# Optimization experiments

Hardware: AMD Instinct MI355X
Metric: run time of the kernel (lower is better)

Reference implementation:

```python
import jax, jax.numpy as jnp
import numpy as np

HID, HEADS, LAYERS = 64, 4, 2
D = HID // HEADS
NU, NE, NV = 30000, 60000, 1000
N_NODES = (NU, NE, NV)
OFFS = (0, NU, NU + NE, NU + NE + NV)
N_TOTAL = NU + NE + NV
# (src_type, dst_type, n_edges); node types: user=0, event=1, venue=2. Order matches module.edge_types.
EDGE_DEFS = (
    (0, 0, 150000),  # friend
    (0, 1, 120000), (0, 1, 60000), (0, 1, 40000), (0, 1, 30000), (0, 1, 50000),  # view/like/save/intent/attend
    (1, 0, 120000), (1, 0, 60000), (1, 0, 40000), (1, 0, 30000), (1, 0, 50000),  # rev_*
    (1, 2, 60000),  # hosted_at
    (2, 1, 60000),  # hosts
)
EDGE_NAMES = ('ei_friend', 'ei_view', 'ei_like', 'ei_save', 'ei_intent', 'ei_attend',
              'ei_rev_view', 'ei_rev_like', 'ei_rev_save', 'ei_rev_intent', 'ei_rev_attend',
              'ei_hosted_at', 'ei_hosts')


def _l2norm(x):
    return x / jnp.maximum(jnp.linalg.norm(x, axis=-1, keepdims=True), 1e-12)


def _hgt_layer(h, edges, Wkqv, bkqv, Wk, Wv, p_rel, Wout, bout, skip):
    # h: list of per-node-type features [N_t, HID]. Fused K/Q/V projection per node type.
    kqv = [h[t] @ Wkqv[t] + bkqv[t] for t in range(3)]  # [N_t, 3*HID]
    k = [a[:, :HID].reshape(-1, HEADS, D) for a in kqv]
    q = [a[:, HID:2 * HID].reshape(-1, HEADS, D) for a in kqv]
    v = [a[:, 2 * HID:].reshape(-1, HEADS, D) for a in kqv]
    scale = 1.0 / np.sqrt(D).astype(np.float32)
    scores, msgs, dsts = [], [], []
    for e, (s, d, _) in enumerate(EDGE_DEFS):
        src_idx, dst_idx = edges[e][0], edges[e][1]
        # per-(edge_type, head) DxD relation transforms (PyG k_rel / v_rel)
        ke = jnp.einsum('nhd,hde->nhe', k[s], Wk[e])[src_idx]  # [E,H,D]
        ve = jnp.einsum('nhd,hde->nhe', v[s], Wv[e])[src_idx]  # [E,H,D]
        qi = q[d][dst_idx]                                      # [E,H,D]
        scores.append((qi * ke).sum(-1) * p_rel[e] * scale)     # [E,H]
        msgs.append(ve)
        dsts.append(dst_idx + OFFS[d])
    sc = jnp.concatenate(scores)   # [E_tot, H]
    ms = jnp.concatenate(msgs)     # [E_tot, H, D]
    dst = jnp.concatenate(dsts)    # [E_tot] global destination ids
    # destination-grouped softmax across all edge types jointly
    smax = jax.lax.stop_gradient(jax.ops.segment_max(sc, dst, num_segments=N_TOTAL))
    ex = jnp.exp(sc - smax[dst])
    den = jax.ops.segment_sum(ex, dst, num_segments=N_TOTAL)
    alpha = ex / den[dst]
    agg = jax.ops.segment_sum(alpha[:, :, None] * ms, dst, num_segments=N_TOTAL).reshape(N_TOTAL, HID)
    out = []
    for t in range(3):
        o = agg[OFFS[t]:OFFS[t + 1]]
        a = jax.nn.gelu(o, approximate=False) @ Wout[t] + bout[t]
        g = jax.nn.sigmoid(skip[t])  # learnable skip gate
        out.append(g * a + (1.0 - g) * h[t])
    return out


def _forward(x_user, x_event, x_venue, W_user, b_user, W_event, b_event, W_venue, b_venue,
             emb_user, emb_event, emb_venue, Wkqv, bkqv, Wk, Wv, p_rel, Wout, bout, skip,
             ids_user, ids_event, ids_venue, edges):
    h = [x_user @ W_user + b_user + emb_user[ids_user],
         x_event @ W_event + b_event + emb_event[ids_event],
         x_venue @ W_venue + b_venue + emb_venue[ids_venue]]
    for l in range(LAYERS):
        h = _hgt_layer(h, edges, Wkqv[l], bkqv[l], Wk[l], Wv[l], p_rel[l], Wout[l], bout[l], skip[l])
        h = [jax.nn.relu(x) for x in h]  # dropout is identity in eval mode
    return tuple(_l2norm(x) for x in h)


def setup_inputs() -> dict:
    key = jax.random.key(0)
    ks = iter(jax.random.split(key, 64))
    s = 0.05
    inp = {
        'x_user': jax.random.normal(next(ks), (NU, 32), jnp.float32),
        'x_event': jax.random.normal(next(ks), (NE, 32), jnp.float32),
        'x_venue': jax.random.normal(next(ks), (NV, 16), jnp.float32),
        'W_user': jax.random.normal(next(ks), (32, HID), jnp.float32) * s,
        'b_user': jnp.zeros((HID,), jnp.float32),
        'W_event': jax.random.normal(next(ks), (32, HID), jnp.float32) * s,
        'b_event': jnp.zeros((HID,), jnp.float32),
        'W_venue': jax.random.normal(next(ks), (16, HID), jnp.float32) * s,
        'b_venue': jnp.zeros((HID,), jnp.float32),
        'emb_user': jax.random.normal(next(ks), (NU, HID), jnp.float32) * s,
        'emb_event': jax.random.normal(next(ks), (NE, HID), jnp.float32) * s,
        'emb_venue': jax.random.normal(next(ks), (NV, HID), jnp.float32) * s,
        'Wkqv': jax.random.normal(next(ks), (LAYERS, 3, HID, 3 * HID), jnp.float32) * s,
        'bkqv': jnp.zeros((LAYERS, 3, 3 * HID), jnp.float32),
        'Wk': jax.random.normal(next(ks), (LAYERS, 13, HEADS, D, D), jnp.float32) * 0.2,
        'Wv': jax.random.normal(next(ks), (LAYERS, 13, HEADS, D, D), jnp.float32) * 0.2,
        'p_rel': jnp.ones((LAYERS, 13, HEADS), jnp.float32),
        'Wout': jax.random.normal(next(ks), (LAYERS, 3, HID, HID), jnp.float32) * s,
        'bout': jnp.zeros((LAYERS, 3, HID), jnp.float32),
        'skip': jnp.ones((LAYERS, 3), jnp.float32),
        'ids_user': jnp.arange(NU, dtype=jnp.int32),
        'ids_event': jnp.arange(NE, dtype=jnp.int32),
        'ids_venue': jnp.arange(NV, dtype=jnp.int32),
    }
    for name, (st, dt, n) in zip(EDGE_NAMES, EDGE_DEFS):
        src = jax.random.randint(next(ks), (n,), 0, N_NODES[st], dtype=jnp.int32)
        dst = jax.random.randint(next(ks), (n,), 0, N_NODES[dt], dtype=jnp.int32)
        inp[name] = jnp.stack([src, dst])
    return inp


def reference(x_user, x_event, x_venue, W_user, b_user, W_event, b_event, W_venue, b_venue,
              emb_user, emb_event, emb_venue, Wkqv, bkqv, Wk, Wv, p_rel, Wout, bout, skip,
              ids_user, ids_event, ids_venue,
              ei_friend, ei_view, ei_like, ei_save, ei_intent, ei_attend,
              ei_rev_view, ei_rev_like, ei_rev_save, ei_rev_intent, ei_rev_attend,
              ei_hosted_at, ei_hosts):
    edges = (ei_friend, ei_view, ei_like, ei_save, ei_intent, ei_attend,
             ei_rev_view, ei_rev_like, ei_rev_save, ei_rev_intent, ei_rev_attend,
             ei_hosted_at, ei_hosts)
    return _forward(x_user, x_event, x_venue, W_user, b_user, W_event, b_event, W_venue, b_venue,
                    emb_user, emb_event, emb_venue, Wkqv, bkqv, Wk, Wv, p_rel, Wout, bout, skip,
                    ids_user, ids_event, ids_venue, edges)
```

## Files before the change

kernel.cpp:

```cpp
#include <hip/hip_runtime.h>
#include <hip/hip_fp16.h>
#include <math.h>

#define HID   64
#define HEADS 4
#define DH    16
#define NU    30000
#define NE_   60000
#define NV    1000
#define NTOT  91000
#define ETOT  870000
#define NSLOT 541000
#define LAYERS 2

__device__ const int d_EOFF[14] = {0,150000,270000,330000,370000,400000,450000,
                                   570000,630000,670000,700000,750000,810000,870000};
__device__ const int d_ECNT[13] = {150000,120000,60000,40000,30000,50000,
                                   120000,60000,40000,30000,50000,60000,60000};
__device__ const int d_EST[13]  = {0,0,0,0,0,0,1,1,1,1,1,1,2};
__device__ const int d_EDT[13]  = {0,1,1,1,1,1,0,0,0,0,0,2,1};
__device__ const int d_NOFF[3]  = {0, NU, NU + NE_};
__device__ const int d_EBASE[13] = {0,30000,60000,90000,120000,150000,
                                    180000,240000,300000,360000,420000,480000,540000};

struct EdgePtrs { const int* p[13]; };

typedef float f32x2 __attribute__((ext_vector_type(2)));

__device__ __forceinline__ void pk_fma(f32x2& acc, f32x2 a, f32x2 b) {
    asm("v_pk_fma_f32 %0, %1, %2, %0" : "+v"(acc) : "v"(a), "v"(b));
}

__device__ __forceinline__ int node_type(int n) {
    return (n >= NU) + (n >= NU + NE_);
}

__global__ void k_init(const float* __restrict__ xu, const float* __restrict__ xe,
                       const float* __restrict__ xv,
                       const float* __restrict__ Wu, const float* __restrict__ bu,
                       const float* __restrict__ We, const float* __restrict__ be,
                       const float* __restrict__ Wv_, const float* __restrict__ bv,
                       const float* __restrict__ embu, const float* __restrict__ embe,
                       const float* __restrict__ embv,
                       const int* __restrict__ idu, const int* __restrict__ ide,
                       const int* __restrict__ idv,
                       float* __restrict__ h) {
    int gid = blockIdx.x * blockDim.x + threadIdx.x;
    if (gid >= NTOT * HID) return;
    int node = gid >> 6, j = gid & 63;
    const float *x, *W, *b, *emb; const int* ids; int in_dim, n;
    if (node < NU)            { n = node;           x = xu; W = Wu;  b = bu; emb = embu; ids = idu; in_dim = 32; }
    else if (node < NU + NE_) { n = node - NU;      x = xe; W = We;  b = be; emb = embe; ids = ide; in_dim = 32; }
    else                      { n = node - NU - NE_;x = xv; W = Wv_; b = bv; emb = embv; ids = idv; in_dim = 16; }
    float acc = b[j] + emb[(size_t)ids[n] * HID + j];
    for (int i = 0; i < in_dim; i++) acc += x[(size_t)n * in_dim + i] * W[i * HID + j];
    h[gid] = acc;
}

__global__ void k_cnt(EdgePtrs ep, int* __restrict__ cnt) {
    int eidx = blockIdx.x * blockDim.x + threadIdx.x;
    if (eidx >= ETOT) return;
    int e = 0;
    #pragma unroll
    for (int i = 1; i < 13; i++) e += (eidx >= d_EOFF[i]);
    int li = eidx - d_EOFF[e];
    int dst = ep.p[e][d_ECNT[e] + li];
    atomicAdd(&cnt[d_NOFF[d_EDT[e]] + dst], 1);
}

__global__ void k_scan_a(const int* __restrict__ cnt, int* __restrict__ partial) {
    __shared__ int s[256];
    int i = blockIdx.x * 256 + threadIdx.x;
    s[threadIdx.x] = (i < NTOT) ? cnt[i] : 0;
    __syncthreads();
    for (int off = 128; off > 0; off >>= 1) {
        if (threadIdx.x < off) s[threadIdx.x] += s[threadIdx.x + off];
        __syncthreads();
    }
    if (threadIdx.x == 0) partial[blockIdx.x] = s[0];
}

__global__ void k_scan_b(int* __restrict__ partial, int nblk) {
    __shared__ int s[512];
    int t = threadIdx.x;
    s[t] = (t < nblk) ? partial[t] : 0;
    __syncthreads();
    for (int off = 1; off < 512; off <<= 1) {
        int v = (t >= off) ? s[t - off] : 0;
        __syncthreads();
        s[t] += v;
        __syncthreads();
    }
    if (t < nblk) partial[t] = t ? s[t - 1] : 0;
}

__global__ void k_scan_c(const int* __restrict__ cnt, const int* __restrict__ partial,
                         int* __restrict__ row_ptr) {
    __shared__ int s[256];
    int i = blockIdx.x * 256 + threadIdx.x, t = threadIdx.x;
    int v = (i < NTOT) ? cnt[i] : 0;
    s[t] = v;
    __syncthreads();
    for (int off = 1; off < 256; off <<= 1) {
        int u = (t >= off) ? s[t - off] : 0;
        __syncthreads();
        s[t] += u;
        __syncthreads();
    }
    if (i < NTOT) row_ptr[i] = s[t] - v + partial[blockIdx.x];
    if (i == NTOT - 1) row_ptr[NTOT] = s[t] + partial[blockIdx.x];
}

__global__ void k_fill(EdgePtrs ep, const int* __restrict__ row_ptr,
                       int* __restrict__ cursor, int* __restrict__ csr) {
    int eidx = blockIdx.x * blockDim.x + threadIdx.x;
    if (eidx >= ETOT) return;
    int e = 0;
    #pragma unroll
    for (int i = 1; i < 13; i++) e += (eidx >= d_EOFF[i]);
    int li = eidx - d_EOFF[e];
    const int* base = ep.p[e];
    int src = base[li], dst = base[d_ECNT[e] + li];
    int dg = d_NOFF[d_EDT[e]] + dst;
    int pos = atomicAdd(&cursor[dg], 1);
    csr[row_ptr[dg] + pos] = d_EBASE[e] + src;
}

__global__ __launch_bounds__(192, 3)
void k_kqvt(const float* __restrict__ h, const float* __restrict__ Wkqv,
            const float* __restrict__ bkqv, const float* __restrict__ Wk,
            const float* __restrict__ Wv, const float* __restrict__ prel,
            float* __restrict__ qagg, __half2* __restrict__ kvt, int layer) {
    int n0 = blockIdx.x * 16;
    int t = node_type(n0);
    __shared__ float hT[64][16];
    __shared__ float kq[16][192];
    int j = threadIdx.x;

    const float* hb = h + (size_t)n0 * 64;
    for (int i = j; i < 256; i += 192) {
        int n = i >> 4, ic = i & 15;
        float4 hv = *(const float4*)(hb + n * 64 + ic * 4);
        hT[ic * 4 + 0][n] = hv.x;
        hT[ic * 4 + 1][n] = hv.y;
        hT[ic * 4 + 2][n] = hv.z;
        hT[ic * 4 + 3][n] = hv.w;
    }
    __syncthreads();

    const float* Wc = Wkqv + (size_t)(layer * 3 + t) * HID * 192 + j;
    float b = bkqv[(layer * 3 + t) * 192 + j];
    f32x2 acc2[8];
    #pragma unroll
    for (int p = 0; p < 8; p++) { acc2[p].x = b; acc2[p].y = b; }
    #pragma unroll
    for (int i = 0; i < 64; i++) {
        float w = Wc[(size_t)i * 192];
        f32x2 wp; wp.x = w; wp.y = w;
        #pragma unroll
        for (int qd = 0; qd < 4; qd++) {
            float4 hv = *(const float4*)(&hT[i][qd * 4]);
            f32x2 p0; p0.x = hv.x; p0.y = hv.y;
            pk_fma(acc2[2 * qd], p0, wp);
            f32x2 p1; p1.x = hv.z; p1.y = hv.w;
            pk_fma(acc2[2 * qd + 1], p1, wp);
        }
    }
    #pragma unroll
    for (int p = 0; p < 8; p++) {
        kq[2 * p][j]     = acc2[p].x;
        kq[2 * p + 1][j] = acc2[p].y;
    }
    if (j >= 64 && j < 128) {
        #pragma unroll
        for (int p = 0; p < 8; p++) {
            if (n0 + 2 * p < NTOT)     qagg[(size_t)(n0 + 2 * p) * 64 + (j - 64)]     = acc2[p].x;
            if (n0 + 2 * p + 1 < NTOT) qagg[(size_t)(n0 + 2 * p + 1) * 64 + (j - 64)] = acc2[p].y;
        }
    }
    __syncthreads();

    int wave = j >> 6, lane = j & 63;
    int hh = lane >> 4, xo = lane & 15;
    int ne = (t == 2) ? 1 : 6;
    int e0 = (t == 0) ? 0 : (t == 1) ? 6 : 12;
    int eA = e0 + wave, eB = e0 + wave + 3;
    bool vA = wave < ne, vB = wave + 3 < ne;
    int nt = n0 - d_NOFF[t];
    f32x2 wkA[8], wvA[8], wkB[8], wvB[8];
    int sbA = 0, sbB = 0;
    if (vA) {
        const float* Wkp = Wk + (((size_t)layer * 13 + eA) * 4 + hh) * 256 + xo;
        const float* Wvp = Wv + (((size_t)layer * 13 + eA) * 4 + hh) * 256 + xo;
        float pr = prel[(layer * 13 + eA) * 4 + hh] * 0.25f;
        #pragma unroll
        for (int p = 0; p < 8; p++) {
            wkA[p].x = Wkp[(2 * p)     * 16] * pr;
            wkA[p].y = Wkp[(2 * p + 1) * 16] * pr;
            wvA[p].x = Wvp[(2 * p)     * 16];
            wvA[p].y = Wvp[(2 * p + 1) * 16];
        }
        sbA = d_EBASE[eA] + nt;
    }
    if (vB) {
        const float* Wkp = Wk + (((size_t)layer * 13 + eB) * 4 + hh) * 256 + xo;
        const float* Wvp = Wv + (((size_t)layer * 13 + eB) * 4 + hh) * 256 + xo;
        float pr = prel[(layer * 13 + eB) * 4 + hh] * 0.25f;
        #pragma unroll
        for (int p = 0; p < 8; p++) {
            wkB[p].x = Wkp[(2 * p)     * 16] * pr;
            wkB[p].y = Wkp[(2 * p + 1) * 16] * pr;
            wvB[p].x = Wvp[(2 * p)     * 16];
            wvB[p].y = Wvp[(2 * p + 1) * 16];
        }
        sbB = d_EBASE[eB] + nt;
    }
    #pragma unroll
    for (int n = 0; n < 16; n++) {
        bool ok = (n0 + n) < NTOT;
        const float* kr = &kq[n][hh * 16];
        const float* vr = &kq[n][128 + hh * 16];
        float4 k0 = ((const float4*)kr)[0];
        float4 k1 = ((const float4*)kr)[1];
        float4 k2 = ((const float4*)kr)[2];
        float4 k3 = ((const float4*)kr)[3];
        float4 v0 = ((const float4*)vr)[0];
        float4 v1 = ((const float4*)vr)[1];
        float4 v2 = ((const float4*)vr)[2];
        float4 v3 = ((const float4*)vr)[3];
        if (vA & ok) {
            f32x2 ak; ak.x = 0.f; ak.y = 0.f;
            f32x2 av; av.x = 0.f; av.y = 0.f;
            f32x2 p0;
            p0.x = k0.x; p0.y = k0.y; pk_fma(ak, p0, wkA[0]);
            p0.x = k0.z; p0.y = k0.w; pk_fma(ak, p0, wkA[1]);
            p0.x = k1.x; p0.y = k1.y; pk_fma(ak, p0, wkA[2]);
            p0.x = k1.z; p0.y = k1.w; pk_fma(ak, p0, wkA[3]);
            p0.x = k2.x; p0.y = k2.y; pk_fma(ak, p0, wkA[4]);
            p0.x = k2.z; p0.y = k2.w; pk_fma(ak, p0, wkA[5]);
            p0.x = k3.x; p0.y = k3.y; pk_fma(ak, p0, wkA[6]);
            p0.x = k3.z; p0.y = k3.w; pk_fma(ak, p0, wkA[7]);
            p0.x = v0.x; p0.y = v0.y; pk_fma(av, p0, wvA[0]);
            p0.x = v0.z; p0.y = v0.w; pk_fma(av, p0, wvA[1]);
            p0.x = v1.x; p0.y = v1.y; pk_fma(av, p0, wvA[2]);
            p0.x = v1.z; p0.y = v1.w; pk_fma(av, p0, wvA[3]);
            p0.x = v2.x; p0.y = v2.y; pk_fma(av, p0, wvA[4]);
            p0.x = v2.z; p0.y = v2.w; pk_fma(av, p0, wvA[5]);
            p0.x = v3.x; p0.y = v3.y; pk_fma(av, p0, wvA[6]);
            p0.x = v3.z; p0.y = v3.w; pk_fma(av, p0, wvA[7]);
            float kt = ak.x + ak.y;
            float vt = av.x + av.y;
            kvt[(size_t)(sbA + n) * 64 + lane] = __float22half2_rn(make_float2(kt, vt));
        }
        if (vB & ok) {
            f32x2 ak; ak.x = 0.f; ak.y = 0.f;
            f32x2 av; av.x = 0.f; av.y = 0.f;
            f32x2 p0;
            p0.x = k0.x; p0.y = k0.y; pk_fma(ak, p0, wkB[0]);
            p0.x = k0.z; p0.y = k0.w; pk_fma(ak, p0, wkB[1]);
            p0.x = k1.x; p0.y = k1.y; pk_fma(ak, p0, wkB[2]);
            p0.x = k1.z; p0.y = k1.w; pk_fma(ak, p0, wkB[3]);
            p0.x = k2.x; p0.y = k2.y; pk_fma(ak, p0, wkB[4]);
            p0.x = k2.z; p0.y = k2.w; pk_fma(ak, p0, wkB[5]);
            p0.x = k3.x; p0.y = k3.y; pk_fma(ak, p0, wkB[6]);
            p0.x = k3.z; p0.y = k3.w; pk_fma(ak, p0, wkB[7]);
            p0.x = v0.x; p0.y = v0.y; pk_fma(av, p0, wvB[0]);
            p0.x = v0.z; p0.y = v0.w; pk_fma(av, p0, wvB[1]);
            p0.x = v1.x; p0.y = v1.y; pk_fma(av, p0, wvB[2]);
            p0.x = v1.z; p0.y = v1.w; pk_fma(av, p0, wvB[3]);
            p0.x = v2.x; p0.y = v2.y; pk_fma(av, p0, wvB[4]);
            p0.x = v2.z; p0.y = v2.w; pk_fma(av, p0, wvB[5]);
            p0.x = v3.x; p0.y = v3.y; pk_fma(av, p0, wvB[6]);
            p0.x = v3.z; p0.y = v3.w; pk_fma(av, p0, wvB[7]);
            float kt = ak.x + ak.y;
            float vt = av.x + av.y;
            kvt[(size_t)(sbB + n) * 64 + lane] = __float22half2_rn(make_float2(kt, vt));
        }
    }
}

__device__ __forceinline__ float row_sum16(float x) {
    int v;
    v = __builtin_amdgcn_update_dpp(0, __float_as_int(x), 0xB1, 0xF, 0xF, true);
    x += __int_as_float(v);
    v = __builtin_amdgcn_update_dpp(0, __float_as_int(x), 0x4E, 0xF, 0xF, true);
    x += __int_as_float(v);
    v = __builtin_amdgcn_update_dpp(0, __float_as_int(x), 0x141, 0xF, 0xF, true);
    x += __int_as_float(v);
    v = __builtin_amdgcn_update_dpp(0, __float_as_int(x), 0x140, 0xF, 0xF, true);
    x += __int_as_float(v);
    return x;
}

__device__ __forceinline__ void osm_step(float s, float vv,
                                         float& m, float& l, float& acc) {
    float d = s - m;
    float t = __expf(-fabsf(d));
    bool pos = d > 0.f;
    m = fmaxf(m, s);
    float sc = pos ? t : 1.f;
    float es = pos ? 1.f : t;
    l   = l * sc + es;
    acc = acc * sc + es * vv;
}

__global__ __launch_bounds__(512)
void k_gather(float* __restrict__ qagg, const __half2* __restrict__ kvt,
              const int* __restrict__ row_ptr, const int* __restrict__ csr) {
    int wave = threadIdx.x >> 6, lane = threadIdx.x & 63;
    int node = blockIdx.x * 8 + wave;
    if (node >= NTOT) return;
    float q = qagg[(size_t)node * 64 + lane];
    int beg = row_ptr[node], end = row_ptr[node + 1];
    float m0 = -1e30f, l0 = 0.f, a0 = 0.f;
    float m1 = -1e30f, l1 = 0.f, a1 = 0.f;
    for (int base = beg; base < end; base += 64) {
        int n = end - base; if (n > 64) n = 64;
        int ent = csr[base + ((lane < n) ? lane : 0)];
        for (int c = 0; c < n; c += 8) {
            int cn = n - c; if (cn > 8) cn = 8;
            __half2 f[8];
            #pragma unroll
            for (int k = 0; k < 8; k++) {
                int idx = c + ((k < cn) ? k : 0);
                int sl = __shfl(ent, idx, 64);
                f[k] = kvt[(size_t)sl * 64 + lane];
            }
            float s8[8];
            #pragma unroll
            for (int k = 0; k < 8; k++) {
                if (k >= cn) break;
                s8[k] = row_sum16(q * __low2float(f[k]));
            }
            #pragma unroll
            for (int k = 0; k < 8; k += 2) {
                if (k < cn)     osm_step(s8[k],   __high2float(f[k]),   m0, l0, a0);
                if (k + 1 < cn) osm_step(s8[k+1], __high2float(f[k+1]), m1, l1, a1);
            }
        }
    }
    float M   = fmaxf(m0, m1);
    float e0  = __expf(m0 - M), e1 = __expf(m1 - M);
    float l   = l0 * e0 + l1 * e1;
    float acc = a0 * e0 + a1 * e1;
    qagg[(size_t)node * 64 + lane] = (l > 0.f) ? acc / l : 0.f;
}

__global__ __launch_bounds__(256)
void k_out(const float* __restrict__ agg, const float* __restrict__ Wout,
           const float* __restrict__ bout, const float* __restrict__ skip,
           float* __restrict__ h, float* __restrict__ out, int layer, int last) {
    int b = blockIdx.x; int t, n0, lim;
    if (b < 938)       { t = 0; n0 = b * 32;                 lim = NU; }
    else if (b < 2813) { t = 1; n0 = NU + (b - 938) * 32;    lim = NU + NE_; }
    else               { t = 2; n0 = NU + NE_ + (b - 2813) * 32; lim = NTOT; }
    int nn = min(32, lim - n0);
    __shared__ float gs[32][64];
    for (int i = threadIdx.x; i < nn * 64; i += 256) {
        float o = agg[(size_t)n0 * 64 + i];
        gs[i >> 6][i & 63] = 0.5f * o * (1.f + erff(o * 0.70710678118654752f));
    }
    __syncthreads();
    int j = threadIdx.x & 63, g = threadIdx.x >> 6;
    const float* W = Wout + (size_t)(layer * 3 + t) * HID * HID;
    float bb = bout[(layer * 3 + t) * HID + j];
    float acc[8];
    #pragma unroll
    for (int n = 0; n < 8; n++) acc[n] = bb;
    for (int i = 0; i < 64; i++) {
        float w = W[i * 64 + j];
        #pragma unroll
        for (int n = 0; n < 8; n++) acc[n] += gs[g * 8 + n][i] * w;
    }
    float gk = 1.f / (1.f + __expf(-skip[layer * 3 + t]));
    #pragma unroll
    for (int n = 0; n < 8; n++) {
        int node = n0 + g * 8 + n;
        if (node >= lim) continue;
        float r = gk * acc[n] + (1.f - gk) * h[(size_t)node * 64 + j];
        r = fmaxf(r, 0.f);
        if (!last) {
            h[(size_t)node * 64 + j] = r;
        } else {
            float ss = r * r;
            ss += __shfl_xor(ss, 1, 64);  ss += __shfl_xor(ss, 2, 64);
            ss += __shfl_xor(ss, 4, 64);  ss += __shfl_xor(ss, 8, 64);
            ss += __shfl_xor(ss, 16, 64); ss += __shfl_xor(ss, 32, 64);
            float nrm = fmaxf(sqrtf(ss), 1e-12f);
            out[(size_t)node * 64 + j] = r / nrm;
        }
    }
}

extern "C" void kernel_launch(void* const* d_in, const int* in_sizes, int n_in,
                              void* d_out, int out_size, void* d_ws, size_t ws_size,
                              hipStream_t stream) {
    const float* xu   = (const float*)d_in[0];
    const float* xe   = (const float*)d_in[1];
    const float* xv   = (const float*)d_in[2];
    const float* Wu   = (const float*)d_in[3];
    const float* bu   = (const float*)d_in[4];
    const float* We   = (const float*)d_in[5];
    const float* be   = (const float*)d_in[6];
    const float* Wv_  = (const float*)d_in[7];
    const float* bv   = (const float*)d_in[8];
    const float* embu = (const float*)d_in[9];
    const float* embe = (const float*)d_in[10];
    const float* embv = (const float*)d_in[11];
    const float* Wkqv = (const float*)d_in[12];
    const float* bkqv = (const float*)d_in[13];
    const float* Wk   = (const float*)d_in[14];
    const float* Wv   = (const float*)d_in[15];
    const float* prel = (const float*)d_in[16];
    const float* Wout = (const float*)d_in[17];
    const float* bout = (const float*)d_in[18];
    const float* skip = (const float*)d_in[19];
    const int*   idu  = (const int*)d_in[20];
    const int*   ide  = (const int*)d_in[21];
    const int*   idv  = (const int*)d_in[22];
    EdgePtrs ep;
    for (int e = 0; e < 13; e++) ep.p[e] = (const int*)d_in[23 + e];

    float* ws  = (float*)d_ws;
    float* h      = ws;
    float* qagg   = h    + (size_t)NTOT * HID;
    __half2* kvt  = (__half2*)(qagg + (size_t)NTOT * HID);
    int* cnt     = (int*)(kvt + (size_t)NSLOT * HID);
    int* cursor  = cnt + NTOT;
    int* row_ptr = cursor + NTOT;
    int* partial = row_ptr + NTOT + 1;
    int* csr     = partial + 512;

    k_init<<<(NTOT * HID + 255) / 256, 256, 0, stream>>>(
        xu, xe, xv, Wu, bu, We, be, Wv_, bv, embu, embe, embv, idu, ide, idv, h);

    hipMemsetAsync(cnt, 0, (size_t)2 * NTOT * 4, stream);
    int nblk = (NTOT + 255) / 256;
    k_cnt<<<(ETOT + 255) / 256, 256, 0, stream>>>(ep, cnt);
    k_scan_a<<<nblk, 256, 0, stream>>>(cnt, partial);
    k_scan_b<<<1, 512, 0, stream>>>(partial, nblk);
    k_scan_c<<<nblk, 256, 0, stream>>>(cnt, partial, row_ptr);
    k_fill<<<(ETOT + 255) / 256, 256, 0, stream>>>(ep, row_ptr, cursor, csr);

    for (int l = 0; l < LAYERS; l++) {
        k_kqvt<<<(NTOT + 15) / 16, 192, 0, stream>>>(h, Wkqv, bkqv, Wk, Wv, prel,
                                                     qagg, kvt, l);
        k_gather<<<(NTOT + 7) / 8, 512, 0, stream>>>(qagg, kvt, row_ptr, csr);
        k_out<<<2845, 256, 0, stream>>>(qagg, Wout, bout, skip, h,
                                        (float*)d_out, l, l == LAYERS - 1);
    }
}
```

Baseline: 686.3 us.

## Tile input projection per 16 nodes and raise occupancy bounds on kqvt and gather

```diff
diff --git a/kernel.cpp b/kernel.cpp
--- a/kernel.cpp
+++ b/kernel.cpp
@@ -35,26 +35,77 @@
     return (n >= NU) + (n >= NU + NE_);
 }
 
-__global__ void k_init(const float* __restrict__ xu, const float* __restrict__ xe,
-                       const float* __restrict__ xv,
-                       const float* __restrict__ Wu, const float* __restrict__ bu,
-                       const float* __restrict__ We, const float* __restrict__ be,
-                       const float* __restrict__ Wv_, const float* __restrict__ bv,
-                       const float* __restrict__ embu, const float* __restrict__ embe,
-                       const float* __restrict__ embv,
-                       const int* __restrict__ idu, const int* __restrict__ ide,
-                       const int* __restrict__ idv,
-                       float* __restrict__ h) {
-    int gid = blockIdx.x * blockDim.x + threadIdx.x;
-    if (gid >= NTOT * HID) return;
-    int node = gid >> 6, j = gid & 63;
-    const float *x, *W, *b, *emb; const int* ids; int in_dim, n;
-    if (node < NU)            { n = node;           x = xu; W = Wu;  b = bu; emb = embu; ids = idu; in_dim = 32; }
-    else if (node < NU + NE_) { n = node - NU;      x = xe; W = We;  b = be; emb = embe; ids = ide; in_dim = 32; }
-    else                      { n = node - NU - NE_;x = xv; W = Wv_; b = bv; emb = embv; ids = idv; in_dim = 16; }
-    float acc = b[j] + emb[(size_t)ids[n] * HID + j];
-    for (int i = 0; i < in_dim; i++) acc += x[(size_t)n * in_dim + i] * W[i * HID + j];
-    h[gid] = acc;
+__global__ __launch_bounds__(64)
+void k_init(const float* __restrict__ xu, const float* __restrict__ xe,
+            const float* __restrict__ xv,
+            const float* __restrict__ Wu, const float* __restrict__ bu,
+            const float* __restrict__ We, const float* __restrict__ be,
+            const float* __restrict__ Wv_, const float* __restrict__ bv,
+            const float* __restrict__ embu, const float* __restrict__ embe,
+            const float* __restrict__ embv,
+            const int* __restrict__ idu, const int* __restrict__ ide,
+            const int* __restrict__ idv,
+            float* __restrict__ h) {
+    int n0 = blockIdx.x * 16;
+    int t = node_type(n0);
+    int j = threadIdx.x;
+    const float *x, *W, *bb, *emb; const int* ids; int in_dim;
+    if (t == 0)      { x = xu; W = Wu;  bb = bu; emb = embu; ids = idu; in_dim = 32; }
+    else if (t == 1) { x = xe; W = We;  bb = be; emb = embe; ids = ide; in_dim = 32; }
+    else             { x = xv; W = Wv_; bb = bv; emb = embv; ids = idv; in_dim = 16; }
+    int nl = n0 - d_NOFF[t];
+    int nn = min(16, NTOT - n0);
+    __shared__ float xT[32][20];
+    int ncs = (in_dim == 32) ? 3 : 2;
+    int nch = 1 << ncs;
+    for (int idx = j; idx < (nch << 4); idx += 64) {
+        int n = idx >> ncs, c = idx & (nch - 1);
+        float4 v = make_float4(0.f, 0.f, 0.f, 0.f);
+        if (n < nn) v = *(const float4*)(x + (size_t)(nl + n) * in_dim + c * 4);
+        xT[c * 4 + 0][n] = v.x;
+        xT[c * 4 + 1][n] = v.y;
+        xT[c * 4 + 2][n] = v.z;
+        xT[c * 4 + 3][n] = v.w;
+    }
+    __syncthreads();
+    float bj = bb[j];
+    f32x2 acc2[8];
+    #pragma unroll
+    for (int p = 0; p < 8; p++) {
+        float ex = (2 * p     < nn) ? emb[(size_t)ids[nl + 2 * p    ] * 64 + j] : 0.f;
+        float ey = (2 * p + 1 < nn) ? emb[(size_t)ids[nl + 2 * p + 1] * 64 + j] : 0.f;
+        acc2[p].x = bj + ex; acc2[p].y = bj + ey;
+    }
+    if (in_dim == 32) {
+        #pragma unroll
+        for (int i = 0; i < 32; i++) {
+            float w = W[i * 64 + j];
+            f32x2 w2; w2.x = w; w2.y = w;
+            #pragma unroll
+            for (int qd = 0; qd < 4; qd++) {
+                float4 hv = *(const float4*)(&xT[i][qd * 4]);
+                f32x2 p0; p0.x = hv.x; p0.y = hv.y; pk_fma(acc2[2 * qd],     p0, w2);
+                f32x2 p1; p1.x = hv.z; p1.y = hv.w; pk_fma(acc2[2 * qd + 1], p1, w2);
+            }
+        }
+    } else {
+        #pragma unroll
+        for (int i = 0; i < 16; i++) {
+            float w = W[i * 64 + j];
+            f32x2 w2; w2.x = w; w2.y = w;
+            #pragma unroll
+            for (int qd = 0; qd < 4; qd++) {
+                float4 hv = *(const float4*)(&xT[i][qd * 4]);
+                f32x2 p0; p0.x = hv.x; p0.y = hv.y; pk_fma(acc2[2 * qd],     p0, w2);
+                f32x2 p1; p1.x = hv.z; p1.y = hv.w; pk_fma(acc2[2 * qd + 1], p1, w2);
+            }
+        }
+    }
+    #pragma unroll
+    for (int p = 0; p < 8; p++) {
+        if (2 * p     < nn) h[(size_t)(n0 + 2 * p)     * 64 + j] = acc2[p].x;
+        if (2 * p + 1 < nn) h[(size_t)(n0 + 2 * p + 1) * 64 + j] = acc2[p].y;
+    }
 }
 
 __global__ void k_cnt(EdgePtrs ep, int* __restrict__ cnt) {
@@ -126,14 +177,14 @@
     csr[row_ptr[dg] + pos] = d_EBASE[e] + src;
 }
 
-__global__ __launch_bounds__(192, 3)
+__global__ __launch_bounds__(192, 6)
 void k_kqvt(const float* __restrict__ h, const float* __restrict__ Wkqv,
             const float* __restrict__ bkqv, const float* __restrict__ Wk,
             const float* __restrict__ Wv, const float* __restrict__ prel,
             float* __restrict__ qagg, __half2* __restrict__ kvt, int layer) {
     int n0 = blockIdx.x * 16;
     int t = node_type(n0);
-    __shared__ float hT[64][16];
+    __shared__ float hT[64][20];
     __shared__ float kq[16][192];
     int j = threadIdx.x;
 
@@ -304,7 +355,7 @@
     acc = acc * sc + es * vv;
 }
 
-__global__ __launch_bounds__(512)
+__global__ __launch_bounds__(512, 8)
 void k_gather(float* __restrict__ qagg, const __half2* __restrict__ kvt,
               const int* __restrict__ row_ptr, const int* __restrict__ csr) {
     int wave = threadIdx.x >> 6, lane = threadIdx.x & 63;
@@ -431,7 +482,7 @@
     int* partial = row_ptr + NTOT + 1;
     int* csr     = partial + 512;
 
-    k_init<<<(NTOT * HID + 255) / 256, 256, 0, stream>>>(
+    k_init<<<(NTOT + 15) / 16, 64, 0, stream>>>(
         xu, xe, xv, Wu, bu, We, be, Wv_, bv, embu, embe, embv, idu, ide, idv, h);
 
     hipMemsetAsync(cnt, 0, (size_t)2 * NTOT * 4, stream);
```

Measured after the change: 1.162 ms. +69.3%, slower.
